# Performance work log

Hardware: AMD Instinct MI355X
Metric: run time of the kernel (lower is better)

The kernel has to match this reference:

```python
import jax, jax.numpy as jnp
import numpy as np

LEAKY = 0.1
VOXEL = 0.25
NSAMPLE = 16
HID = 8                      # PositionalEncodingFourier hidden_dim
SCALE = 2.0 * np.pi
TEMP = 10000.0


def _bn(x, g, b, eps):
    # eval-mode BatchNorm1d of a freshly-built module: running_mean=0, running_var=1
    return x * (g / jnp.sqrt(1.0 + eps)) + b


def _knn(k, q, r):
    # q [B,N,3], r [B,M,3] -> [B,N,k] indices of k nearest points of r
    d = (jnp.sum(q * q, -1)[:, :, None] + jnp.sum(r * r, -1)[:, None, :]
         - 2.0 * jnp.einsum('bnc,bmc->bnm', q, r))
    return jax.lax.top_k(-d, k)[1]


def _group(p, idx):
    # p [B,M,C], idx [B,N,K] -> [B,N,K,C]  (grouping_operation / index_points_group)
    return jax.vmap(lambda pp, ii: pp[ii])(p, idx)


def _pec(pe, w, b):
    # pe [M,3] (columns treated as z,y,x), max_len=(1,1,1)
    emb = pe / (1.0 + 1e-6) * SCALE
    dim_t = TEMP ** (2.0 * (jnp.arange(HID) // 2) / HID)          # [HID]
    p = emb[:, :, None] / dim_t                                    # [M,3,HID]
    pos = jnp.stack([jnp.sin(p[:, :, 0::2]), jnp.cos(p[:, :, 1::2])], -1)  # [M,3,HID/2,2]
    return pos.reshape(pe.shape[0], 3 * HID) @ w + b               # [M,64]


def _ipc(pos_diff, P):
    # IntraPatchCost: pos_diff [B,3,S,N] -> local softmax attention over S: [B,N,S]
    B, _, S, N = pos_diff.shape
    pd = pos_diff.transpose(0, 3, 2, 1).reshape(B * N, S, 3)
    dv = jnp.round(pd / VOXEL)
    x = jax.nn.relu(_bn(pd @ P['ie_w1'] + P['ie_b1'], P['ie_g'], P['ie_bt'], 1e-5))
    x = x @ P['ie_w2'] + P['ie_b2']                                # [BN,S,64]
    pe_raw = ((pd - dv * VOXEL) / VOXEL).reshape(-1, 3)
    x = x + _pec(pe_raw, P['pec_w'], P['pec_b']).reshape(B * N, S, -1)
    h = jax.nn.relu(_bn(x @ P['pm_w1'] + P['pm_b1'], P['pm_g1'], P['pm_bt1'], 1e-3))
    h = jax.nn.relu(_bn(h @ P['pm_w2'] + P['pm_b2'], P['pm_g2'], P['pm_bt2'], 1e-3))
    h = _bn(h @ P['pm_w3'] + P['pm_b3'], P['pm_g3'], P['pm_bt3'], 1e-3)
    h = _bn(h @ P['pm_w4'] + P['pm_b4'], P['pm_g4'], P['pm_bt4'], 1e-3)  # [BN,S,1]
    return jax.nn.softmax(h[..., 0], -1).reshape(B, N, S)


def setup_inputs():
    key = jax.random.key(0)
    ks = iter(jax.random.split(key, 64))
    rn = lambda shape, s=1.0: jax.random.normal(next(ks), shape, jnp.float32) * s
    B, N, D = 2, 8192, 64
    inp = {
        'xyz1': rn((B, 3, N)), 'xyz2': rn((B, 3, N)), 'xyz2w': rn((B, 3, N)),
        'points1': rn((B, D, N)), 'points2': rn((B, D, N)), 'sf': rn((B, 3, N), 0.1),
    }
    for c, cin in (('1', 2 * D), ('2', 2 * D), ('3', 64 + 3), ('4', 2 * 64)):
        inp['cw' + c + 'a'] = rn((cin, 64), 0.1)
        inp['cb' + c + 'a'] = jnp.zeros((64,), jnp.float32)
        inp['cw' + c + 'b'] = rn((64, 64), 0.1)
        inp['cb' + c + 'b'] = jnp.zeros((64,), jnp.float32)
    inp.update(ie_w1=rn((3, 64), 0.1), ie_b1=jnp.zeros((64,), jnp.float32),
               ie_g=jnp.ones((64,), jnp.float32), ie_bt=jnp.zeros((64,), jnp.float32),
               ie_w2=rn((64, 64), 0.1), ie_b2=jnp.zeros((64,), jnp.float32),
               pec_w=rn((24, 64), 0.1), pec_b=jnp.zeros((64,), jnp.float32))
    for i, (cin, cout) in enumerate([(64, 64), (64, 64), (64, 32), (32, 1)], 1):
        inp['pm_w%d' % i] = rn((cin, cout), 0.1)
        inp['pm_b%d' % i] = jnp.zeros((cout,), jnp.float32)
        inp['pm_g%d' % i] = jnp.ones((cout,), jnp.float32)
        inp['pm_bt%d' % i] = jnp.zeros((cout,), jnp.float32)
    return inp


def reference(xyz1, xyz2, xyz2w, points1, points2, sf,
              cw1a, cb1a, cw1b, cb1b, cw2a, cb2a, cw2b, cb2b,
              cw3a, cb3a, cw3b, cb3b, cw4a, cb4a, cw4b, cb4b,
              ie_w1, ie_b1, ie_g, ie_bt, ie_w2, ie_b2, pec_w, pec_b,
              pm_w1, pm_b1, pm_g1, pm_bt1, pm_w2, pm_b2, pm_g2, pm_bt2,
              pm_w3, pm_b3, pm_g3, pm_bt3, pm_w4, pm_b4, pm_g4, pm_bt4):
    P = dict(ie_w1=ie_w1, ie_b1=ie_b1, ie_g=ie_g, ie_bt=ie_bt, ie_w2=ie_w2, ie_b2=ie_b2,
             pec_w=pec_w, pec_b=pec_b,
             pm_w1=pm_w1, pm_b1=pm_b1, pm_g1=pm_g1, pm_bt1=pm_bt1,
             pm_w2=pm_w2, pm_b2=pm_b2, pm_g2=pm_g2, pm_bt2=pm_bt2,
             pm_w3=pm_w3, pm_b3=pm_b3, pm_g3=pm_g3, pm_bt3=pm_bt3,
             pm_w4=pm_w4, pm_b4=pm_b4, pm_g4=pm_g4, pm_bt4=pm_bt4)
    x1 = xyz1.transpose(0, 2, 1)     # [B,N,3]
    x2 = xyz2.transpose(0, 2, 1)
    x2w = xyz2w.transpose(0, 2, 1)
    p1 = points1.transpose(0, 2, 1)  # [B,N,D]
    p2 = points2.transpose(0, 2, 1)
    sg = jax.lax.stop_gradient       # pointutils.knn is non-differentiable
    idx = _knn(NSAMPLE, sg(x1 + sf.transpose(0, 2, 1)), sg(x2))
    idxw = _knn(NSAMPLE, sg(x1), sg(x2w))
    dir_xyz = _group(x2, idx) - x1[:, :, None, :]    # [B,N,K,3]
    dir_xyzw = _group(x2, idxw) - x1[:, :, None, :]
    gp2 = _group(p2, idx)                            # [B,N,K,D]
    gp2w = _group(p2, idxw)
    gp1 = jnp.broadcast_to(p1[:, :, None, :], gp2.shape)
    act = lambda t: jax.nn.leaky_relu(t, LEAKY)
    chain = lambda t, wa, ba, wb, bb: act(act(t @ wa + ba) @ wb + bb)
    f1 = chain(jnp.concatenate([gp1, gp2], -1), cw1a, cb1a, cw1b, cb1b)    # [B,N,K,64]
    f2 = chain(jnp.concatenate([gp1, gp2w], -1), cw2a, cb2a, cw2b, cb2b)
    attn = _ipc(dir_xyz.transpose(0, 3, 2, 1), P)    # [B,N,K]
    attnw = _ipc(dir_xyzw.transpose(0, 3, 2, 1), P)
    costA = jnp.einsum('bnk,bnkc->bnc', attn, f1)
    f3 = chain(jnp.concatenate([dir_xyzw, f2], -1), cw3a, cb3a, cw3b, cb3b)
    costB = jnp.einsum('bnk,bnkc->bnc', attnw, f3)
    out = chain(jnp.concatenate([costA, costB], -1), cw4a, cb4a, cw4b, cb4b)  # [B,N,64]
    return out.transpose(0, 2, 1)    # [B,64,N]
```

## Files before the change

### kernel.cpp

```cpp
#include <hip/hip_runtime.h>
#include <hip/hip_bf16.h>
#include <math.h>

typedef __hip_bfloat16 bf16;

#define NPTS  8192
#define BATCH 2
#define KNB   16
#define NPART 16
#define PARTC (NPTS / NPART)
#define CAP   24
#define BN    (BATCH * NPTS)

#define C_IE 0.9999950000374997f
#define C_PM 0.9995003746877732f

enum {
  WOFF_CW1A = 0,     WOFF_CB1A = 8192,  WOFF_CW1B = 8256,  WOFF_CB1B = 12352,
  WOFF_CW2A = 12416, WOFF_CB2A = 20608, WOFF_CW2B = 20672, WOFF_CB2B = 24768,
  WOFF_CW3A = 24832, WOFF_CB3A = 29120, WOFF_CW3B = 29184, WOFF_CB3B = 33280,
  WOFF_CW4A = 33344, WOFF_CB4A = 41536, WOFF_CW4B = 41600, WOFF_CB4B = 45696,
  WOFF_IEW1 = 45760, WOFF_IEB1 = 45952, WOFF_IEG  = 46016, WOFF_IEBT = 46080,
  WOFF_IEW2 = 46144, WOFF_IEB2 = 50240, WOFF_PECW = 50304, WOFF_PECB = 51840,
  WOFF_PMW1 = 51904, WOFF_PMB1 = 56000, WOFF_PMG1 = 56064, WOFF_PMT1 = 56128,
  WOFF_PMW2 = 56192, WOFF_PMB2 = 60288, WOFF_PMG2 = 60352, WOFF_PMT2 = 60416,
  WOFF_PMW3 = 60480, WOFF_PMB3 = 62528, WOFF_PMG3 = 62560, WOFF_PMT3 = 62592,
  WOFF_PMW4 = 62624, WOFF_PMB4 = 62656, WOFF_PMG4 = 62657, WOFF_PMT4 = 62658
};

#define BOFF_W    0u
#define BOFF_FLAG 262144u
#define BOFF_PK   262160u
#define BOFF_WB   1310736u
#define BOFF_IDX  2359312u
#define BOFF_AW   4456464u
#define BOFF_P1T  5505040u
#define BOFF_P2T  9699344u
#define BOFF_PART BOFF_P1T

typedef __attribute__((ext_vector_type(4))) float f32x4;
typedef __attribute__((ext_vector_type(8))) short bf16x8;
typedef __attribute__((ext_vector_type(4))) unsigned int u32x4;

__device__ __forceinline__ float lrelu(float v) { return v > 0.f ? v : 0.1f * v; }

__device__ __forceinline__ float ldin(const void* p, size_t i, int f32) {
  return f32 ? ((const float*)p)[i] : __bfloat162float(((const bf16*)p)[i]);
}
__device__ __forceinline__ void stout(void* p, size_t i, float v, int f32) {
  if (f32) ((float*)p)[i] = v;
  else ((bf16*)p)[i] = __float2bfloat16(v);
}

__device__ __forceinline__ unsigned int bf16rne(float x) {
  unsigned int u = __float_as_uint(x);
  return (u + 0x7fffu + ((u >> 16) & 1u)) >> 16;
}
__device__ __forceinline__ void splitbf(float x, unsigned int& h, unsigned int& l) {
  h = bf16rne(x);
  float hf = __uint_as_float(h << 16);
  l = bf16rne(x - hf);
}
__device__ __forceinline__ unsigned int packbf(float v) {
  unsigned int h, lo;
  splitbf(v, h, lo);
  return h | (lo << 16);
}

__device__ __forceinline__ void insert16(float d, int id, float* best, int* bidx) {
#pragma unroll
  for (int p = 0; p < KNB; ++p) {
    bool c = d < best[p];
    float tb = best[p]; int ti = bidx[p];
    best[p] = c ? d : tb; bidx[p] = c ? id : ti;
    d = c ? tb : d; id = c ? ti : id;
  }
}

#define BPASS(arr, J, K) \
  _Pragma("unroll") \
  for (int i = 0; i < 16; ++i) { \
    int ix = i ^ (J); \
    if (ix > i) { \
      float lo = fminf(arr[i], arr[ix]); \
      float hi = fmaxf(arr[i], arr[ix]); \
      if ((i & (K)) == 0) { arr[i] = lo; arr[ix] = hi; } \
      else { arr[i] = hi; arr[ix] = lo; } \
    } \
  }

__device__ __forceinline__ float qsq(float4 qv) {
  return __fadd_rn(__fadd_rn(__fmul_rn(qv.x, qv.x), __fmul_rn(qv.y, qv.y)),
                   __fmul_rn(qv.z, qv.z));
}
__device__ __forceinline__ float refdist(float4 qv, float sq, float4 rv) {
  float sr = qsq(rv);
  float dot = __fmaf_rn(qv.z, rv.z, __fmaf_rn(qv.y, rv.y, __fmul_rn(qv.x, rv.x)));
  return __fsub_rn(__fadd_rn(sq, sr), __fadd_rn(dot, dot));
}
__device__ __forceinline__ float refdist_sr(float4 qv, float sq, float4 rv) {
  float dot = __fmaf_rn(qv.z, rv.z, __fmaf_rn(qv.y, rv.y, __fmul_rn(qv.x, rv.x)));
  return __fsub_rn(__fadd_rn(sq, rv.w), __fadd_rn(dot, dot));
}

__global__ void k_detect(const void* __restrict__ pts1, int* __restrict__ flag) {
  int tid = threadIdx.x;
  const bf16* p = (const bf16*)pts1;
  int cnt = 0;
  for (int i = tid; i < 1024; i += 64) {
    float v = __bfloat162float(p[i]);
    if (!(fabsf(v) <= 64.f)) cnt++;
  }
#pragma unroll
  for (int s = 32; s; s >>= 1) cnt += __shfl_down(cnt, s);
  if (tid == 0) *flag = (cnt >= 8) ? 1 : 0;
}

struct PrepTab {
  const void* src[40];
  int off[40];
  int n[40];
  float scale[40];
};

__global__ void k_prep(PrepTab tab, float* __restrict__ W, const int* __restrict__ flag) {
  int f32 = *flag;
  int a = blockIdx.x;
  const void* s = tab.src[a];
  float* d = W + tab.off[a];
  float sc = tab.scale[a];
  for (int i = threadIdx.x; i < tab.n[a]; i += blockDim.x) d[i] = ldin(s, i, f32) * sc;
}

struct WTab { int woff[16]; int nn[16]; int kreal[16]; int mode[16]; int fb[16]; int nm; };

__global__ __launch_bounds__(64) void k_wbprep(WTab wt, const float* __restrict__ W,
                                               unsigned int* __restrict__ WB) {
  int f = blockIdx.x, l = threadIdx.x;
  int m = 0;
  for (int i = 1; i < wt.nm; ++i)
    if (wt.fb[i] <= f) m = i;
  int ntile = wt.nn[m] >> 4;
  int local = f - wt.fb[m];
  int ks = local / ntile, nt = local - ks * ntile;
  int g = l >> 4, c = l & 15;
  int col = nt * 16 + c;
  int N = wt.nn[m], kr = wt.kreal[m], wo = wt.woff[m], mode = wt.mode[m];
  unsigned int hw[4], lw[4];
#pragma unroll
  for (int r = 0; r < 4; ++r) {
    float wv2[2];
#pragma unroll
    for (int e = 0; e < 2; ++e) {
      int k = ks * 32 + g * 8 + 2 * r + e;
      int srck;
      if (mode == 1) srck = (k < 64) ? k + 3 : ((k < 67) ? k - 64 : -1);
      else srck = (k < kr) ? k : -1;
      wv2[e] = (srck >= 0) ? W[wo + srck * N + col] : 0.f;
    }
    unsigned int h0, l0, h1, l1;
    splitbf(wv2[0], h0, l0);
    splitbf(wv2[1], h1, l1);
    hw[r] = h0 | (h1 << 16);
    lw[r] = l0 | (l1 << 16);
  }
  unsigned int* d = WB + ((size_t)f * 64 + l) * 8;
  d[0] = hw[0]; d[1] = hw[1]; d[2] = hw[2]; d[3] = hw[3];
  d[4] = lw[0]; d[5] = lw[1]; d[6] = lw[2]; d[7] = lw[3];
}

__global__ void k_pack(const void* __restrict__ xyz1, const void* __restrict__ xyz2,
                       const void* __restrict__ xyz2w, const void* __restrict__ sf,
                       float4* __restrict__ pk, const int* __restrict__ flag) {
  int f32 = *flag;
  int t = blockIdx.x * 256 + threadIdx.x;
  int b = t >> 13, n = t & (NPTS - 1);
  size_t base = (size_t)b * 3 * NPTS + n;
  float ax = ldin(xyz1, base, f32), ay = ldin(xyz1, base + NPTS, f32), az = ldin(xyz1, base + 2 * NPTS, f32);
  float sx = ldin(sf, base, f32),   sy = ldin(sf, base + NPTS, f32),   sz = ldin(sf, base + 2 * NPTS, f32);
  float4 p0 = make_float4(__fadd_rn(ax, sx), __fadd_rn(ay, sy), __fadd_rn(az, sz), 0.f);
  p0.w = qsq(p0);
  float4 p1 = make_float4(ax, ay, az, 0.f);
  p1.w = qsq(p1);
  float4 p2 = make_float4(ldin(xyz2, base, f32), ldin(xyz2, base + NPTS, f32), ldin(xyz2, base + 2 * NPTS, f32), 0.f);
  p2.w = qsq(p2);
  float4 p3 = make_float4(ldin(xyz2w, base, f32), ldin(xyz2w, base + NPTS, f32), ldin(xyz2w, base + 2 * NPTS, f32), 0.f);
  p3.w = qsq(p3);
  pk[t]          = p0;
  pk[t + BN]     = p1;
  pk[t + 2 * BN] = p2;
  pk[t + 3 * BN] = p3;
}

__global__ __launch_bounds__(64) void k_tr(const void* __restrict__ src,
                                           unsigned int* __restrict__ dst,
                                           const int* __restrict__ flag) {
  __shared__ float tile[64][65];
  int f32 = *flag;
  int tid = threadIdx.x;
  int n0 = blockIdx.x * 64;
  int b = blockIdx.y;
  for (int i = 0; i < 64; ++i)
    tile[i][tid] = ldin(src, ((size_t)b * 64 + i) * NPTS + n0 + tid, f32);
  __syncthreads();
  for (int i = 0; i < 64; ++i)
    dst[((size_t)b * NPTS + n0 + i) * 64 + tid] = packbf(tile[tid][i]);
}

__global__ __launch_bounds__(256) void k_knnp(const float4* __restrict__ pk,
                                              unsigned short* __restrict__ part_idx) {
  __shared__ unsigned short sbuf[256 * CAP];
  int tid = threadIdx.x;
  int n = blockIdx.x * 256 + tid;
  int b = blockIdx.y;
  int which = blockIdx.z >> 4;
  int part  = blockIdx.z & 15;
  const float4* q = pk + (size_t)which * BN;
  const float4* r = pk + (size_t)(2 + which) * BN + (size_t)b * NPTS;
  float4 qv = q[b * NPTS + n];
  float sq = qsq(qv);

  float best[KNB];
#pragma unroll
  for (int p = 0; p < KNB; ++p) best[p] = 3.4e38f;

  const int c0 = part * PARTC;
  for (int t = 0; t < PARTC / 16; ++t) {
    const float4* rr = r + c0 + t * 16;
    float fr[16];
#pragma unroll
    for (int j = 0; j < 16; ++j) fr[j] = refdist_sr(qv, sq, rr[j]);
    BPASS(fr, 1, 2)
    BPASS(fr, 2, 4) BPASS(fr, 1, 4)
    BPASS(fr, 4, 8) BPASS(fr, 2, 8) BPASS(fr, 1, 8)
    BPASS(fr, 8, 16) BPASS(fr, 4, 16) BPASS(fr, 2, 16) BPASS(fr, 1, 16)
#pragma unroll
    for (int i = 0; i < 16; ++i) best[i] = fminf(best[i], fr[15 - i]);
    BPASS(best, 8, 16) BPASS(best, 4, 16) BPASS(best, 2, 16) BPASS(best, 1, 16)
  }
  float thr = best[KNB - 1];

  int cnt = 0;
  for (int t = 0; t < PARTC / 16; ++t) {
    const float4* rr = r + c0 + t * 16;
#pragma unroll
    for (int j = 0; j < 16; ++j) {
      float dd = refdist_sr(qv, sq, rr[j]);
      if (dd <= thr && cnt < CAP) {
        sbuf[tid * CAP + cnt] = (unsigned short)(c0 + t * 16 + j);
        cnt++;
      }
    }
  }

  float bd[KNB]; int bi[KNB];
#pragma unroll
  for (int p = 0; p < KNB; ++p) { bd[p] = 3.4e38f; bi[p] = 0; }
  for (int m = 0; m < CAP; ++m) {
    if (m < cnt) {
      int id = sbuf[tid * CAP + m];
      float dd = refdist(qv, sq, r[id]);
      insert16(dd, id, bd, bi);
    }
  }
  size_t o = ((((size_t)which * BATCH + b) * NPART + part) * NPTS + n) * KNB;
#pragma unroll
  for (int p = 0; p < KNB; ++p) part_idx[o + p] = (unsigned short)bi[p];
}

__global__ void k_merge(const float4* __restrict__ pk,
                        const unsigned short* __restrict__ part_idx,
                        int* __restrict__ idxf) {
  int t = blockIdx.x * 256 + threadIdx.x;
  int n = t & (NPTS - 1);
  int wb = t >> 13;
  int b = wb & (BATCH - 1);
  int which = wb / BATCH;
  const float4* q = pk + (size_t)which * BN;
  const float4* r = pk + (size_t)(2 + which) * BN + (size_t)b * NPTS;
  float4 qv = q[b * NPTS + n];
  float sq = qsq(qv);
  float best[KNB]; int bidx[KNB];
#pragma unroll
  for (int p = 0; p < KNB; ++p) { best[p] = 3.4e38f; bidx[p] = 0; }
  for (int part = 0; part < NPART; ++part) {
    size_t o = ((((size_t)which * BATCH + b) * NPART + part) * NPTS + n) * KNB;
#pragma unroll
    for (int m = 0; m < KNB; ++m) {
      int id = part_idx[o + m];
      float dd = refdist(qv, sq, r[id]);
      if (dd < best[KNB - 1]) insert16(dd, id, best, bidx);
    }
  }
  size_t oo = (size_t)t * KNB;
#pragma unroll
  for (int p = 0; p < KNB; ++p) idxf[oo + p] = bidx[p];
}

__device__ __forceinline__ bf16x8 mk8(unsigned int w0, unsigned int w1,
                                      unsigned int w2, unsigned int w3) {
  u32x4 u;
  u.x = w0; u.y = w1; u.z = w2; u.w = w3;
  return __builtin_bit_cast(bf16x8, u);
}

__device__ __forceinline__ void mkA_pk(u32x4 qa, u32x4 qb, bf16x8& ah, bf16x8& al) {
  unsigned int q0 = qa.x, q1 = qa.y, q2 = qa.z, q3 = qa.w;
  unsigned int q4 = qb.x, q5 = qb.y, q6 = qb.z, q7 = qb.w;
  ah = mk8((q0 & 0xffffu) | (q1 << 16), (q2 & 0xffffu) | (q3 << 16),
           (q4 & 0xffffu) | (q5 << 16), (q6 & 0xffffu) | (q7 << 16));
  al = mk8((q0 >> 16) | (q1 & 0xffff0000u), (q2 >> 16) | (q3 & 0xffff0000u),
           (q4 >> 16) | (q5 & 0xffff0000u), (q6 >> 16) | (q7 & 0xffff0000u));
}
__device__ __forceinline__ void mkA_lds(const unsigned int* p, bf16x8& ah, bf16x8& al) {
  mkA_pk(*(const u32x4*)p, *(const u32x4*)(p + 4), ah, al);
}

#define FRAG_IEW2 0
#define FRAG_PECW 8
#define FRAG_PMW1 12
#define FRAG_PMW2 20
#define FRAG_PMW3 28
#define FRAG_C1A  32
#define FRAG_C1B  48
#define FRAG_C2A  56
#define FRAG_C2B  72
#define FRAG_C3A  80
#define FRAG_C3B  92
#define FRAG_C4A  100
#define FRAG_C4B  116
#define NFRAG     124

__device__ __forceinline__ f32x4 mfma_bb(bf16x8 ah, bf16x8 al,
                                         const unsigned int* __restrict__ WB,
                                         int f, int lane, f32x4 acc) {
  const u32x4* p = (const u32x4*)WB + ((size_t)(f * 64 + lane)) * 2;
  u32x4 h4 = p[0], l4 = p[1];
  bf16x8 bh = __builtin_bit_cast(bf16x8, h4);
  bf16x8 bl = __builtin_bit_cast(bf16x8, l4);
  acc = __builtin_amdgcn_mfma_f32_16x16x32_bf16(al, bh, acc, 0, 0, 0);
  acc = __builtin_amdgcn_mfma_f32_16x16x32_bf16(ah, bl, acc, 0, 0, 0);
  acc = __builtin_amdgcn_mfma_f32_16x16x32_bf16(ah, bh, acc, 0, 0, 0);
  return acc;
}

__device__ __forceinline__ void layer64(const unsigned int* __restrict__ xp,
                                        const unsigned int* __restrict__ WB,
                                        int fbase, int lane, f32x4 acc[4]) {
  int c = lane & 15, g = lane >> 4;
  bf16x8 ah0, al0, ah1, al1;
  mkA_lds(xp + c * 68 + g * 8, ah0, al0);
  mkA_lds(xp + c * 68 + 32 + g * 8, ah1, al1);
#pragma unroll
  for (int nt = 0; nt < 4; ++nt) {
    acc[nt] = mfma_bb(ah0, al0, WB, fbase + nt, lane, acc[nt]);
    acc[nt] = mfma_bb(ah1, al1, WB, fbase + 4 + nt, lane, acc[nt]);
  }
}

__device__ __forceinline__ void epi_pack(int lane, f32x4 acc[4], unsigned int* xp,
                                         const float* gw, const float* bw, bool relu) {
  int c = lane & 15, g = lane >> 4;
#pragma unroll
  for (int nt = 0; nt < 4; ++nt) {
    float gv = gw ? gw[nt * 16 + c] : 1.f;
    float bv = gw ? bw[nt * 16 + c] : 0.f;
#pragma unroll
    for (int r = 0; r < 4; ++r) {
      float v = acc[nt][r];
      if (gw) v = fmaf(v, gv, bv);
      if (relu) v = fmaxf(v, 0.f);
      xp[(g * 4 + r) * 68 + nt * 16 + c] = packbf(v);
    }
  }
}

__device__ __forceinline__ void epi_lrelu(int lane, f32x4 acc[4], unsigned int* xp) {
  int c = lane & 15, g = lane >> 4;
#pragma unroll
  for (int nt = 0; nt < 4; ++nt) {
#pragma unroll
    for (int r = 0; r < 4; ++r)
      xp[(g * 4 + r) * 68 + nt * 16 + c] = packbf(lrelu(acc[nt][r]));
  }
}

__global__ __launch_bounds__(256, 3) void k_logit(const float* __restrict__ W,
                                                  const unsigned int* __restrict__ WB,
                                                  const int* __restrict__ idxf,
                                                  const float4* __restrict__ pk,
                                                  unsigned short* __restrict__ AW) {
  __shared__ unsigned int xp_s[4][16 * 68];
  __shared__ unsigned int tg_s[4][16 * 36];
  const int l = threadIdx.x & 63;
  const int wv = threadIdx.x >> 6;
  const int c = l & 15, g = l >> 4;
  unsigned int* xp = xp_s[wv];
  unsigned int* tg = tg_s[wv];
  const int which = blockIdx.y;
  const int pt = blockIdx.x * 4 + wv;
  const int n = pt & (NPTS - 1);
  const int b = pt >> 13;

  int idxv = idxf[(((size_t)which * BATCH + b) * NPTS + n) * KNB + c];
  float4 pv = pk[(size_t)2 * BN + (size_t)b * NPTS + idxv];
  float4 qp = pk[(size_t)BN + pt];
  float pdx = pv.x - qp.x, pdy = pv.y - qp.y, pdz = pv.z - qp.z;

  {
    unsigned int* tr = tg + c * 36;
#pragma unroll
    for (int j = 0; j < 3; ++j) {
      int t = g * 3 + j;
      int c3 = t >> 2, fq = t & 3;
      float pdc = (c3 == 0) ? pdx : (c3 == 1) ? pdy : pdz;
      float pe = (pdc - rintf(pdc * 4.f) * 0.25f) * 4.f;
      float tt = pe / 1.000001f * 6.28318530717958647692f;
      float dv = (fq == 0) ? 1.f : (fq == 1) ? 10.f : (fq == 2) ? 100.f : 1000.f;
      float sn, cs;
      sincosf(tt / dv, &sn, &cs);
      unsigned int hs, ls2, hc, lc;
      splitbf(sn, hs, ls2);
      splitbf(cs, hc, lc);
      tr[2 * t] = hs | (ls2 << 16);
      tr[2 * t + 1] = hc | (lc << 16);
    }
    if (g == 3) {
#pragma unroll
      for (int z = 24; z < 32; ++z) tr[z] = 0u;
    }
  }

  {
    unsigned int* xr = xp + c * 68 + g * 16;
#pragma unroll
    for (int m4 = 0; m4 < 4; ++m4) {
      int ch = g * 16 + m4 * 4;
      float4 bb = *(const float4*)(W + WOFF_IEB1 + ch);
      float4 w0 = *(const float4*)(W + WOFF_IEW1 + ch);
      float4 w1 = *(const float4*)(W + WOFF_IEW1 + 64 + ch);
      float4 w2 = *(const float4*)(W + WOFF_IEW1 + 128 + ch);
      float4 gg = *(const float4*)(W + WOFF_IEG + ch);
      float4 bt = *(const float4*)(W + WOFF_IEBT + ch);
      float v0 = fmaf(pdz, w2.x, fmaf(pdy, w1.x, fmaf(pdx, w0.x, bb.x)));
      float v1 = fmaf(pdz, w2.y, fmaf(pdy, w1.y, fmaf(pdx, w0.y, bb.y)));
      float v2 = fmaf(pdz, w2.z, fmaf(pdy, w1.z, fmaf(pdx, w0.z, bb.z)));
      float v3 = fmaf(pdz, w2.w, fmaf(pdy, w1.w, fmaf(pdx, w0.w, bb.w)));
      v0 = fmaxf(fmaf(v0, gg.x, bt.x), 0.f);
      v1 = fmaxf(fmaf(v1, gg.y, bt.y), 0.f);
      v2 = fmaxf(fmaf(v2, gg.z, bt.z), 0.f);
      v3 = fmaxf(fmaf(v3, gg.w, bt.w), 0.f);
      u32x4 pk4;
      pk4.x = packbf(v0); pk4.y = packbf(v1);
      pk4.z = packbf(v2); pk4.w = packbf(v3);
      *(u32x4*)(xr + m4 * 4) = pk4;
    }
  }
  __builtin_amdgcn_wave_barrier();

  f32x4 acc[4];
#pragma unroll
  for (int nt = 0; nt < 4; ++nt) {
    float bs = W[WOFF_IEB2 + nt * 16 + c] + W[WOFF_PECB + nt * 16 + c];
    acc[nt].x = bs; acc[nt].y = bs; acc[nt].z = bs; acc[nt].w = bs;
  }
  layer64(xp, WB, FRAG_IEW2, l, acc);
  {
    bf16x8 ah, al;
    mkA_lds(tg + c * 36 + g * 8, ah, al);
#pragma unroll
    for (int nt = 0; nt < 4; ++nt)
      acc[nt] = mfma_bb(ah, al, WB, FRAG_PECW + nt, l, acc[nt]);
  }
  __builtin_amdgcn_wave_barrier();
  epi_pack(l, acc, xp, nullptr, nullptr, false);
  __builtin_amdgcn_wave_barrier();

#pragma unroll
  for (int nt = 0; nt < 4; ++nt) {
    float bs = W[WOFF_PMB1 + nt * 16 + c];
    acc[nt].x = bs; acc[nt].y = bs; acc[nt].z = bs; acc[nt].w = bs;
  }
  layer64(xp, WB, FRAG_PMW1, l, acc);
  __builtin_amdgcn_wave_barrier();
  epi_pack(l, acc, xp, W + WOFF_PMG1, W + WOFF_PMT1, true);
  __builtin_amdgcn_wave_barrier();

#pragma unroll
  for (int nt = 0; nt < 4; ++nt) {
    float bs = W[WOFF_PMB2 + nt * 16 + c];
    acc[nt].x = bs; acc[nt].y = bs; acc[nt].z = bs; acc[nt].w = bs;
  }
  layer64(xp, WB, FRAG_PMW2, l, acc);
  __builtin_amdgcn_wave_barrier();
  epi_pack(l, acc, xp, W + WOFF_PMG2, W + WOFF_PMT2, true);
  __builtin_amdgcn_wave_barrier();

  f32x4 a3[2];
#pragma unroll
  for (int nt = 0; nt < 2; ++nt) {
    float bs = W[WOFF_PMB3 + nt * 16 + c];
    a3[nt].x = bs; a3[nt].y = bs; a3[nt].z = bs; a3[nt].w = bs;
  }
  {
    bf16x8 ah0, al0, ah1, al1;
    mkA_lds(xp + c * 68 + g * 8, ah0, al0);
    mkA_lds(xp + c * 68 + 32 + g * 8, ah1, al1);
#pragma unroll
    for (int nt = 0; nt < 2; ++nt) {
      a3[nt] = mfma_bb(ah0, al0, WB, FRAG_PMW3 + nt, l, a3[nt]);
      a3[nt] = mfma_bb(ah1, al1, WB, FRAG_PMW3 + 2 + nt, l, a3[nt]);
    }
  }
#pragma unroll
  for (int nt = 0; nt < 2; ++nt) {
    float gv = W[WOFF_PMG3 + nt * 16 + c];
    float bv = W[WOFF_PMT3 + nt * 16 + c];
#pragma unroll
    for (int r = 0; r < 4; ++r) a3[nt][r] = fmaf(a3[nt][r], gv, bv);
  }

  float w4a = W[WOFF_PMW4 + c];
  float w4b = W[WOFF_PMW4 + 16 + c];
  f32x4 pr;
#pragma unroll
  for (int r = 0; r < 4; ++r) pr[r] = fmaf(a3[1][r], w4b, a3[0][r] * w4a);
#pragma unroll
  for (int s = 1; s < 16; s <<= 1) {
#pragma unroll
    for (int r = 0; r < 4; ++r) pr[r] += __shfl_xor(pr[r], s);
  }
  float b4 = W[WOFF_PMB4], g4 = W[WOFF_PMG4], t4 = W[WOFF_PMT4];
  f32x4 lg;
#pragma unroll
  for (int r = 0; r < 4; ++r) lg[r] = fmaf(pr[r] + b4, g4, t4);

  float m = fmaxf(fmaxf(lg[0], lg[1]), fmaxf(lg[2], lg[3]));
#pragma unroll
  for (int s = 16; s < 64; s <<= 1) m = fmaxf(m, __shfl_xor(m, s));
  f32x4 e;
  float ssum = 0.f;
#pragma unroll
  for (int r = 0; r < 4; ++r) { e[r] = expf(lg[r] - m); ssum += e[r]; }
#pragma unroll
  for (int s = 16; s < 64; s <<= 1) ssum += __shfl_xor(ssum, s);
  if (c < 4) {
    int k = g * 4 + c;
    float ev = (c == 0) ? e[0] : (c == 1) ? e[1] : (c == 2) ? e[2] : e[3];
    float aw = ev / ssum;
    AW[(((size_t)which * BATCH + b) * NPTS + n) * KNB + k] =
        (unsigned short)__float2uint_rn(aw * 65535.f);
  }
}

__global__ __launch_bounds__(256, 3) void k_feat(const unsigned int* __restrict__ P1T,
                                                 const unsigned int* __restrict__ P2T,
                                                 const float* __restrict__ W,
                                                 const unsigned int* __restrict__ WB,
                                                 const int* __restrict__ idxf,
                                                 const unsigned short* __restrict__ AW,
                                                 const float4* __restrict__ pk,
                                                 void* __restrict__ out,
                                                 const int* __restrict__ flag) {
  __shared__ unsigned int xp_s[4][16 * 68];
  __shared__ unsigned int costb[4][132];
  __shared__ unsigned int u4b[4][68];
  __shared__ float awb[4][16];
  const int l = threadIdx.x & 63;
  const int wv = threadIdx.x >> 6;
  const int c = l & 15, g = l >> 4;
  unsigned int* xp = xp_s[wv];
  const int f32 = *flag;
  const int pt = blockIdx.x * 4 + wv;
  const int n = pt & (NPTS - 1);
  const int b = pt >> 13;
  float4 qp = pk[(size_t)BN + pt];
  u32x4 z4;
  z4.x = 0u; z4.y = 0u; z4.z = 0u; z4.w = 0u;

  bf16x8 p1h[2], p1l[2];
  {
    const unsigned int* pr = P1T + ((size_t)b * NPTS + n) * 64;
#pragma unroll
    for (int ks = 0; ks < 2; ++ks) {
      u32x4 qa = *(const u32x4*)(pr + ks * 32 + g * 8);
      u32x4 qb = *(const u32x4*)(pr + ks * 32 + g * 8 + 4);
      mkA_pk(qa, qb, p1h[ks], p1l[ks]);
    }
  }

  for (int which = 0; which < 2; ++which) {
    int idxv = idxf[(((size_t)which * BATCH + b) * NPTS + n) * KNB + c];
    float4 pv = pk[(size_t)2 * BN + (size_t)b * NPTS + idxv];
    float pdx = pv.x - qp.x, pdy = pv.y - qp.y, pdz = pv.z - qp.z;
    float aw = (float)AW[(((size_t)which * BATCH + b) * NPTS + n) * KNB + c] *
               (1.f / 65535.f);
    if (g == 0) awb[wv][c] = aw;

    bf16x8 p2h[2], p2l[2];
    {
      const unsigned int* qr = P2T + ((size_t)b * NPTS + idxv) * 64;
#pragma unroll
      for (int ks = 0; ks < 2; ++ks) {
        u32x4 qa = *(const u32x4*)(qr + ks * 32 + g * 8);
        u32x4 qb = *(const u32x4*)(qr + ks * 32 + g * 8 + 4);
        mkA_pk(qa, qb, p2h[ks], p2l[ks]);
      }
    }

    f32x4 acc[4];
    {
      const float* Ba = W + (which == 0 ? WOFF_CB1A : WOFF_CB2A);
      int fa = (which == 0) ? FRAG_C1A : FRAG_C2A;
#pragma unroll
      for (int nt = 0; nt < 4; ++nt) {
        float bs = Ba[nt * 16 + c];
        acc[nt].x = bs; acc[nt].y = bs; acc[nt].z = bs; acc[nt].w = bs;
      }
#pragma unroll
      for (int nt = 0; nt < 4; ++nt) {
        acc[nt] = mfma_bb(p1h[0], p1l[0], WB, fa + nt, l, acc[nt]);
        acc[nt] = mfma_bb(p1h[1], p1l[1], WB, fa + 4 + nt, l, acc[nt]);
        acc[nt] = mfma_bb(p2h[0], p2l[0], WB, fa + 8 + nt, l, acc[nt]);
        acc[nt] = mfma_bb(p2h[1], p2l[1], WB, fa + 12 + nt, l, acc[nt]);
      }
    }
    __builtin_amdgcn_wave_barrier();
    epi_lrelu(l, acc, xp);
    __builtin_amdgcn_wave_barrier();

    {
      const float* Bb = W + (which == 0 ? WOFF_CB1B : WOFF_CB2B);
      int fb = (which == 0) ? FRAG_C1B : FRAG_C2B;
      bf16x8 ah0, al0, ah1, al1;
      mkA_lds(xp + c * 68 + g * 8, ah0, al0);
      mkA_lds(xp + c * 68 + 32 + g * 8, ah1, al1);
#pragma unroll
      for (int nt = 0; nt < 4; ++nt) {
        float bs = Bb[nt * 16 + c];
        acc[nt].x = bs; acc[nt].y = bs; acc[nt].z = bs; acc[nt].w = bs;
        acc[nt] = mfma_bb(ah0, al0, WB, fb + nt, l, acc[nt]);
        acc[nt] = mfma_bb(ah1, al1, WB, fb + 4 + nt, l, acc[nt]);
      }
    }
    __builtin_amdgcn_wave_barrier();

    if (which == 1) {
      epi_lrelu(l, acc, xp);
      if (g == 0) {
        xp[c * 68 + 64] = packbf(pdx);
        xp[c * 68 + 65] = packbf(pdy);
        xp[c * 68 + 66] = packbf(pdz);
        xp[c * 68 + 67] = 0u;
      }
      __builtin_amdgcn_wave_barrier();
      {
        bf16x8 ah0, al0, ah1, al1, ah2, al2;
        mkA_lds(xp + c * 68 + g * 8, ah0, al0);
        mkA_lds(xp + c * 68 + 32 + g * 8, ah1, al1);
        u32x4 qa3 = z4;
        if (g == 0) qa3 = *(const u32x4*)(xp + c * 68 + 64);
        mkA_pk(qa3, z4, ah2, al2);
#pragma unroll
        for (int nt = 0; nt < 4; ++nt) {
          float bs = W[WOFF_CB3A + nt * 16 + c];
          acc[nt].x = bs; acc[nt].y = bs; acc[nt].z = bs; acc[nt].w = bs;
          acc[nt] = mfma_bb(ah0, al0, WB, FRAG_C3A + nt, l, acc[nt]);
          acc[nt] = mfma_bb(ah1, al1, WB, FRAG_C3A + 4 + nt, l, acc[nt]);
          acc[nt] = mfma_bb(ah2, al2, WB, FRAG_C3A + 8 + nt, l, acc[nt]);
        }
      }
      __builtin_amdgcn_wave_barrier();
      epi_lrelu(l, acc, xp);
      __builtin_amdgcn_wave_barrier();
      {
        bf16x8 ah0, al0, ah1, al1;
        mkA_lds(xp + c * 68 + g * 8, ah0, al0);
        mkA_lds(xp + c * 68 + 32 + g * 8, ah1, al1);
#pragma unroll
        for (int nt = 0; nt < 4; ++nt) {
          float bs = W[WOFF_CB3B + nt * 16 + c];
          acc[nt].x = bs; acc[nt].y = bs; acc[nt].z = bs; acc[nt].w = bs;
          acc[nt] = mfma_bb(ah0, al0, WB, FRAG_C3B + nt, l, acc[nt]);
          acc[nt] = mfma_bb(ah1, al1, WB, FRAG_C3B + 4 + nt, l, acc[nt]);
        }
      }
      __builtin_amdgcn_wave_barrier();
    }

    {
      float4 a4r = *(const float4*)&awb[wv][g * 4];
#pragma unroll
      for (int nt = 0; nt < 4; ++nt) {
        float s = lrelu(acc[nt][0]) * a4r.x;
        s = fmaf(lrelu(acc[nt][1]), a4r.y, s);
        s = fmaf(lrelu(acc[nt][2]), a4r.z, s);
        s = fmaf(lrelu(acc[nt][3]), a4r.w, s);
        s += __shfl_xor(s, 16);
        s += __shfl_xor(s, 32);
        if (g == 0) costb[wv][which * 64 + nt * 16 + c] = packbf(s);
      }
    }
  }
  __syncthreads();

  f32x4 a4;
  {
    float bs = W[WOFF_CB4A + wv * 16 + c];
    a4.x = bs; a4.y = bs; a4.z = bs; a4.w = bs;
#pragma unroll
    for (int ks = 0; ks < 4; ++ks) {
      u32x4 qa = z4, qb = z4;
      if (c < 4) {
        qa = *(const u32x4*)(&costb[c][ks * 32 + g * 8]);
        qb = *(const u32x4*)(&costb[c][ks * 32 + g * 8 + 4]);
      }
      bf16x8 ah, al;
      mkA_pk(qa, qb, ah, al);
      a4 = mfma_bb(ah, al, WB, FRAG_C4A + ks * 4 + wv, l, a4);
    }
  }
  if (g == 0) {
#pragma unroll
    for (int r = 0; r < 4; ++r) u4b[r][wv * 16 + c] = packbf(lrelu(a4[r]));
  }
  __syncthreads();

  {
    float bs = W[WOFF_CB4B + wv * 16 + c];
    a4.x = bs; a4.y = bs; a4.z = bs; a4.w = bs;
#pragma unroll
    for (int ks = 0; ks < 2; ++ks) {
      u32x4 qa = z4, qb = z4;
      if (c < 4) {
        qa = *(const u32x4*)(&u4b[c][ks * 32 + g * 8]);
        qb = *(const u32x4*)(&u4b[c][ks * 32 + g * 8 + 4]);
      }
      bf16x8 ah, al;
      mkA_pk(qa, qb, ah, al);
      a4 = mfma_bb(ah, al, WB, FRAG_C4B + ks * 4 + wv, l, a4);
    }
  }
  if (g == 0) {
    int n0 = (blockIdx.x * 4) & (NPTS - 1);
    int b0 = (blockIdx.x * 4) >> 13;
    size_t ob = (size_t)b0 * 64 * NPTS + (size_t)(wv * 16 + c) * NPTS + n0;
#pragma unroll
    for (int r = 0; r < 4; ++r) stout(out, ob + r, lrelu(a4[r]), f32);
  }
}

extern "C" void kernel_launch(void* const* d_in, const int* in_sizes, int n_in,
                              void* d_out, int out_size, void* d_ws, size_t ws_size,
                              hipStream_t stream) {
  (void)in_sizes; (void)n_in; (void)out_size; (void)ws_size;
  float*  W    = (float*)d_ws;
  int*    FLAG = (int*)((char*)d_ws + BOFF_FLAG);
  float4* PK   = (float4*)((char*)d_ws + BOFF_PK);
  unsigned int* WBu = (unsigned int*)((char*)d_ws + BOFF_WB);
  int*    IDX  = (int*)((char*)d_ws + BOFF_IDX);
  unsigned short* AW = (unsigned short*)((char*)d_ws + BOFF_AW);
  unsigned int* P1T = (unsigned int*)((char*)d_ws + BOFF_P1T);
  unsigned int* P2T = (unsigned int*)((char*)d_ws + BOFF_P2T);
  unsigned short* PART = (unsigned short*)((char*)d_ws + BOFF_PART);

  static const int WOFFS[40] = {
    WOFF_CW1A, WOFF_CB1A, WOFF_CW1B, WOFF_CB1B,
    WOFF_CW2A, WOFF_CB2A, WOFF_CW2B, WOFF_CB2B,
    WOFF_CW3A, WOFF_CB3A, WOFF_CW3B, WOFF_CB3B,
    WOFF_CW4A, WOFF_CB4A, WOFF_CW4B, WOFF_CB4B,
    WOFF_IEW1, WOFF_IEB1, WOFF_IEG,  WOFF_IEBT,
    WOFF_IEW2, WOFF_IEB2, WOFF_PECW, WOFF_PECB,
    WOFF_PMW1, WOFF_PMB1, WOFF_PMG1, WOFF_PMT1,
    WOFF_PMW2, WOFF_PMB2, WOFF_PMG2, WOFF_PMT2,
    WOFF_PMW3, WOFF_PMB3, WOFF_PMG3, WOFF_PMT3,
    WOFF_PMW4, WOFF_PMB4, WOFF_PMG4, WOFF_PMT4};
  static const int WNS[40] = {
    8192, 64, 4096, 64,  8192, 64, 4096, 64,  4288, 64, 4096, 64,
    8192, 64, 4096, 64,  192, 64, 64, 64,  4096, 64,  1536, 64,
    4096, 64, 64, 64,  4096, 64, 64, 64,  2048, 32, 32, 32,  32, 1, 1, 1};

  PrepTab tab;
  for (int a = 0; a < 40; ++a) {
    tab.src[a] = d_in[6 + a];
    tab.off[a] = WOFFS[a];
    tab.n[a] = WNS[a];
    tab.scale[a] = 1.f;
  }
  tab.scale[18] = C_IE;
  tab.scale[26] = C_PM; tab.scale[30] = C_PM;
  tab.scale[34] = C_PM; tab.scale[38] = C_PM;

  WTab wt;
  {
    int f = 0, m = 0;
    auto add = [&](int woff, int N, int nks, int kreal, int mode) {
      wt.woff[m] = woff; wt.nn[m] = N; wt.kreal[m] = kreal;
      wt.mode[m] = mode; wt.fb[m] = f;
      f += nks * (N / 16); ++m;
    };
    add(WOFF_IEW2, 64, 2, 64, 0);
    add(WOFF_PECW, 64, 1, 24, 0);
    add(WOFF_PMW1, 64, 2, 64, 0);
    add(WOFF_PMW2, 64, 2, 64, 0);
    add(WOFF_PMW3, 32, 2, 64, 0);
    add(WOFF_CW1A, 64, 4, 128, 0);
    add(WOFF_CW1B, 64, 2, 64, 0);
    add(WOFF_CW2A, 64, 4, 128, 0);
    add(WOFF_CW2B, 64, 2, 64, 0);
    add(WOFF_CW3A, 64, 3, 67, 1);
    add(WOFF_CW3B, 64, 2, 64, 0);
    add(WOFF_CW4A, 64, 4, 128, 0);
    add(WOFF_CW4B, 64, 2, 64, 0);
    wt.nm = m;
  }

  k_detect<<<dim3(1), dim3(64), 0, stream>>>(d_in[3], FLAG);
  k_prep<<<dim3(40), dim3(256), 0, stream>>>(tab, W, FLAG);
  k_wbprep<<<dim3(NFRAG), dim3(64), 0, stream>>>(wt, W, WBu);
  k_pack<<<dim3(64), dim3(256), 0, stream>>>(d_in[0], d_in[1], d_in[2], d_in[5], PK, FLAG);
  k_knnp<<<dim3(NPTS / 256, BATCH, 2 * NPART), dim3(256), 0, stream>>>(PK, PART);
  k_merge<<<dim3(2 * BN / 256), dim3(256), 0, stream>>>(PK, PART, IDX);
  k_tr<<<dim3(NPTS / 64, BATCH), dim3(64), 0, stream>>>(d_in[3], P1T, FLAG);
  k_tr<<<dim3(NPTS / 64, BATCH), dim3(64), 0, stream>>>(d_in[4], P2T, FLAG);
  k_logit<<<dim3(BN / 4, 2), dim3(256), 0, stream>>>(W, WBu, IDX, PK, AW);
  k_feat<<<dim3(BN / 4), dim3(256), 0, stream>>>(P1T, P2T, W, WBu, IDX, AW, PK, d_out, FLAG);
}
```

Measured before the change: 809.4 us.

## Fuse attention-logit MLP and softmax into feature kernel, drop AW buffer

Moves the intra-patch cost MLP and softmax from the separate k_logit kernel into k_feat's per-branch loop, so attention weights stay in registers and are used directly for the weighted sum. This removes one kernel launch, the quantized 16-bit AW global write/read round trip, and the redundant neighbor index/position loads. It also drops the 16-bit quantization of the attention weights. The cost is higher register and LDS pressure in k_feat (extra tg_s buffer), which may lower occupancy under the (256,3) launch bounds.

```diff
diff --git a/kernel.cpp b/kernel.cpp
--- a/kernel.cpp
+++ b/kernel.cpp
@@ -385,191 +385,23 @@
   }
 }
 
-__global__ __launch_bounds__(256, 3) void k_logit(const float* __restrict__ W,
-                                                  const unsigned int* __restrict__ WB,
-                                                  const int* __restrict__ idxf,
-                                                  const float4* __restrict__ pk,
-                                                  unsigned short* __restrict__ AW) {
+__global__ __launch_bounds__(256, 3) void k_feat(const unsigned int* __restrict__ P1T,
+                                                 const unsigned int* __restrict__ P2T,
+                                                 const float* __restrict__ W,
+                                                 const unsigned int* __restrict__ WB,
+                                                 const int* __restrict__ idxf,
+                                                 const float4* __restrict__ pk,
+                                                 void* __restrict__ out,
+                                                 const int* __restrict__ flag) {
   __shared__ unsigned int xp_s[4][16 * 68];
   __shared__ unsigned int tg_s[4][16 * 36];
+  __shared__ unsigned int costb[4][132];
+  __shared__ unsigned int u4b[4][68];
   const int l = threadIdx.x & 63;
   const int wv = threadIdx.x >> 6;
   const int c = l & 15, g = l >> 4;
   unsigned int* xp = xp_s[wv];
   unsigned int* tg = tg_s[wv];
-  const int which = blockIdx.y;
-  const int pt = blockIdx.x * 4 + wv;
-  const int n = pt & (NPTS - 1);
-  const int b = pt >> 13;
-
-  int idxv = idxf[(((size_t)which * BATCH + b) * NPTS + n) * KNB + c];
-  float4 pv = pk[(size_t)2 * BN + (size_t)b * NPTS + idxv];
-  float4 qp = pk[(size_t)BN + pt];
-  float pdx = pv.x - qp.x, pdy = pv.y - qp.y, pdz = pv.z - qp.z;
-
-  {
-    unsigned int* tr = tg + c * 36;
-#pragma unroll
-    for (int j = 0; j < 3; ++j) {
-      int t = g * 3 + j;
-      int c3 = t >> 2, fq = t & 3;
-      float pdc = (c3 == 0) ? pdx : (c3 == 1) ? pdy : pdz;
-      float pe = (pdc - rintf(pdc * 4.f) * 0.25f) * 4.f;
-      float tt = pe / 1.000001f * 6.28318530717958647692f;
-      float dv = (fq == 0) ? 1.f : (fq == 1) ? 10.f : (fq == 2) ? 100.f : 1000.f;
-      float sn, cs;
-      sincosf(tt / dv, &sn, &cs);
-      unsigned int hs, ls2, hc, lc;
-      splitbf(sn, hs, ls2);
-      splitbf(cs, hc, lc);
-      tr[2 * t] = hs | (ls2 << 16);
-      tr[2 * t + 1] = hc | (lc << 16);
-    }
-    if (g == 3) {
-#pragma unroll
-      for (int z = 24; z < 32; ++z) tr[z] = 0u;
-    }
-  }
-
-  {
-    unsigned int* xr = xp + c * 68 + g * 16;
-#pragma unroll
-    for (int m4 = 0; m4 < 4; ++m4) {
-      int ch = g * 16 + m4 * 4;
-      float4 bb = *(const float4*)(W + WOFF_IEB1 + ch);
-      float4 w0 = *(const float4*)(W + WOFF_IEW1 + ch);
-      float4 w1 = *(const float4*)(W + WOFF_IEW1 + 64 + ch);
-      float4 w2 = *(const float4*)(W + WOFF_IEW1 + 128 + ch);
-      float4 gg = *(const float4*)(W + WOFF_IEG + ch);
-      float4 bt = *(const float4*)(W + WOFF_IEBT + ch);
-      float v0 = fmaf(pdz, w2.x, fmaf(pdy, w1.x, fmaf(pdx, w0.x, bb.x)));
-      float v1 = fmaf(pdz, w2.y, fmaf(pdy, w1.y, fmaf(pdx, w0.y, bb.y)));
-      float v2 = fmaf(pdz, w2.z, fmaf(pdy, w1.z, fmaf(pdx, w0.z, bb.z)));
-      float v3 = fmaf(pdz, w2.w, fmaf(pdy, w1.w, fmaf(pdx, w0.w, bb.w)));
-      v0 = fmaxf(fmaf(v0, gg.x, bt.x), 0.f);
-      v1 = fmaxf(fmaf(v1, gg.y, bt.y), 0.f);
-      v2 = fmaxf(fmaf(v2, gg.z, bt.z), 0.f);
-      v3 = fmaxf(fmaf(v3, gg.w, bt.w), 0.f);
-      u32x4 pk4;
-      pk4.x = packbf(v0); pk4.y = packbf(v1);
-      pk4.z = packbf(v2); pk4.w = packbf(v3);
-      *(u32x4*)(xr + m4 * 4) = pk4;
-    }
-  }
-  __builtin_amdgcn_wave_barrier();
-
-  f32x4 acc[4];
-#pragma unroll
-  for (int nt = 0; nt < 4; ++nt) {
-    float bs = W[WOFF_IEB2 + nt * 16 + c] + W[WOFF_PECB + nt * 16 + c];
-    acc[nt].x = bs; acc[nt].y = bs; acc[nt].z = bs; acc[nt].w = bs;
-  }
-  layer64(xp, WB, FRAG_IEW2, l, acc);
-  {
-    bf16x8 ah, al;
-    mkA_lds(tg + c * 36 + g * 8, ah, al);
-#pragma unroll
-    for (int nt = 0; nt < 4; ++nt)
-      acc[nt] = mfma_bb(ah, al, WB, FRAG_PECW + nt, l, acc[nt]);
-  }
-  __builtin_amdgcn_wave_barrier();
-  epi_pack(l, acc, xp, nullptr, nullptr, false);
-  __builtin_amdgcn_wave_barrier();
-
-#pragma unroll
-  for (int nt = 0; nt < 4; ++nt) {
-    float bs = W[WOFF_PMB1 + nt * 16 + c];
-    acc[nt].x = bs; acc[nt].y = bs; acc[nt].z = bs; acc[nt].w = bs;
-  }
-  layer64(xp, WB, FRAG_PMW1, l, acc);
-  __builtin_amdgcn_wave_barrier();
-  epi_pack(l, acc, xp, W + WOFF_PMG1, W + WOFF_PMT1, true);
-  __builtin_amdgcn_wave_barrier();
-
-#pragma unroll
-  for (int nt = 0; nt < 4; ++nt) {
-    float bs = W[WOFF_PMB2 + nt * 16 + c];
-    acc[nt].x = bs; acc[nt].y = bs; acc[nt].z = bs; acc[nt].w = bs;
-  }
-  layer64(xp, WB, FRAG_PMW2, l, acc);
-  __builtin_amdgcn_wave_barrier();
-  epi_pack(l, acc, xp, W + WOFF_PMG2, W + WOFF_PMT2, true);
-  __builtin_amdgcn_wave_barrier();
-
-  f32x4 a3[2];
-#pragma unroll
-  for (int nt = 0; nt < 2; ++nt) {
-    float bs = W[WOFF_PMB3 + nt * 16 + c];
-    a3[nt].x = bs; a3[nt].y = bs; a3[nt].z = bs; a3[nt].w = bs;
-  }
-  {
-    bf16x8 ah0, al0, ah1, al1;
-    mkA_lds(xp + c * 68 + g * 8, ah0, al0);
-    mkA_lds(xp + c * 68 + 32 + g * 8, ah1, al1);
-#pragma unroll
-    for (int nt = 0; nt < 2; ++nt) {
-      a3[nt] = mfma_bb(ah0, al0, WB, FRAG_PMW3 + nt, l, a3[nt]);
-      a3[nt] = mfma_bb(ah1, al1, WB, FRAG_PMW3 + 2 + nt, l, a3[nt]);
-    }
-  }
-#pragma unroll
-  for (int nt = 0; nt < 2; ++nt) {
-    float gv = W[WOFF_PMG3 + nt * 16 + c];
-    float bv = W[WOFF_PMT3 + nt * 16 + c];
-#pragma unroll
-    for (int r = 0; r < 4; ++r) a3[nt][r] = fmaf(a3[nt][r], gv, bv);
-  }
-
-  float w4a = W[WOFF_PMW4 + c];
-  float w4b = W[WOFF_PMW4 + 16 + c];
-  f32x4 pr;
-#pragma unroll
-  for (int r = 0; r < 4; ++r) pr[r] = fmaf(a3[1][r], w4b, a3[0][r] * w4a);
-#pragma unroll
-  for (int s = 1; s < 16; s <<= 1) {
-#pragma unroll
-    for (int r = 0; r < 4; ++r) pr[r] += __shfl_xor(pr[r], s);
-  }
-  float b4 = W[WOFF_PMB4], g4 = W[WOFF_PMG4], t4 = W[WOFF_PMT4];
-  f32x4 lg;
-#pragma unroll
-  for (int r = 0; r < 4; ++r) lg[r] = fmaf(pr[r] + b4, g4, t4);
-
-  float m = fmaxf(fmaxf(lg[0], lg[1]), fmaxf(lg[2], lg[3]));
-#pragma unroll
-  for (int s = 16; s < 64; s <<= 1) m = fmaxf(m, __shfl_xor(m, s));
-  f32x4 e;
-  float ssum = 0.f;
-#pragma unroll
-  for (int r = 0; r < 4; ++r) { e[r] = expf(lg[r] - m); ssum += e[r]; }
-#pragma unroll
-  for (int s = 16; s < 64; s <<= 1) ssum += __shfl_xor(ssum, s);
-  if (c < 4) {
-    int k = g * 4 + c;
-    float ev = (c == 0) ? e[0] : (c == 1) ? e[1] : (c == 2) ? e[2] : e[3];
-    float aw = ev / ssum;
-    AW[(((size_t)which * BATCH + b) * NPTS + n) * KNB + k] =
-        (unsigned short)__float2uint_rn(aw * 65535.f);
-  }
-}
-
-__global__ __launch_bounds__(256, 3) void k_feat(const unsigned int* __restrict__ P1T,
-                                                 const unsigned int* __restrict__ P2T,
-                                                 const float* __restrict__ W,
-                                                 const unsigned int* __restrict__ WB,
-                                                 const int* __restrict__ idxf,
-                                                 const unsigned short* __restrict__ AW,
-                                                 const float4* __restrict__ pk,
-                                                 void* __restrict__ out,
-                                                 const int* __restrict__ flag) {
-  __shared__ unsigned int xp_s[4][16 * 68];
-  __shared__ unsigned int costb[4][132];
-  __shared__ unsigned int u4b[4][68];
-  __shared__ float awb[4][16];
-  const int l = threadIdx.x & 63;
-  const int wv = threadIdx.x >> 6;
-  const int c = l & 15, g = l >> 4;
-  unsigned int* xp = xp_s[wv];
   const int f32 = *flag;
   const int pt = blockIdx.x * 4 + wv;
   const int n = pt & (NPTS - 1);
@@ -593,9 +425,150 @@
     int idxv = idxf[(((size_t)which * BATCH + b) * NPTS + n) * KNB + c];
     float4 pv = pk[(size_t)2 * BN + (size_t)b * NPTS + idxv];
     float pdx = pv.x - qp.x, pdy = pv.y - qp.y, pdz = pv.z - qp.z;
-    float aw = (float)AW[(((size_t)which * BATCH + b) * NPTS + n) * KNB + c] *
-               (1.f / 65535.f);
-    if (g == 0) awb[wv][c] = aw;
+
+    {
+      unsigned int* tr = tg + c * 36;
+#pragma unroll
+      for (int j = 0; j < 3; ++j) {
+        int t = g * 3 + j;
+        int c3 = t >> 2, fq = t & 3;
+        float pdc = (c3 == 0) ? pdx : (c3 == 1) ? pdy : pdz;
+        float pe = (pdc - rintf(pdc * 4.f) * 0.25f) * 4.f;
+        float tt = pe / 1.000001f * 6.28318530717958647692f;
+        float dv = (fq == 0) ? 1.f : (fq == 1) ? 10.f : (fq == 2) ? 100.f : 1000.f;
+        float sn, cs;
+        sincosf(tt / dv, &sn, &cs);
+        unsigned int hs, ls2, hc, lc;
+        splitbf(sn, hs, ls2);
+        splitbf(cs, hc, lc);
+        tr[2 * t] = hs | (ls2 << 16);
+        tr[2 * t + 1] = hc | (lc << 16);
+      }
+      if (g == 3) {
+#pragma unroll
+        for (int z = 24; z < 32; ++z) tr[z] = 0u;
+      }
+    }
+
+    {
+      unsigned int* xr = xp + c * 68 + g * 16;
+#pragma unroll
+      for (int m4 = 0; m4 < 4; ++m4) {
+        int ch = g * 16 + m4 * 4;
+        float4 bb = *(const float4*)(W + WOFF_IEB1 + ch);
+        float4 w0 = *(const float4*)(W + WOFF_IEW1 + ch);
+        float4 w1 = *(const float4*)(W + WOFF_IEW1 + 64 + ch);
+        float4 w2 = *(const float4*)(W + WOFF_IEW1 + 128 + ch);
+        float4 gg = *(const float4*)(W + WOFF_IEG + ch);
+        float4 bt = *(const float4*)(W + WOFF_IEBT + ch);
+        float v0 = fmaf(pdz, w2.x, fmaf(pdy, w1.x, fmaf(pdx, w0.x, bb.x)));
+        float v1 = fmaf(pdz, w2.y, fmaf(pdy, w1.y, fmaf(pdx, w0.y, bb.y)));
+        float v2 = fmaf(pdz, w2.z, fmaf(pdy, w1.z, fmaf(pdx, w0.z, bb.z)));
+        float v3 = fmaf(pdz, w2.w, fmaf(pdy, w1.w, fmaf(pdx, w0.w, bb.w)));
+        v0 = fmaxf(fmaf(v0, gg.x, bt.x), 0.f);
+        v1 = fmaxf(fmaf(v1, gg.y, bt.y), 0.f);
+        v2 = fmaxf(fmaf(v2, gg.z, bt.z), 0.f);
+        v3 = fmaxf(fmaf(v3, gg.w, bt.w), 0.f);
+        u32x4 pk4;
+        pk4.x = packbf(v0); pk4.y = packbf(v1);
+        pk4.z = packbf(v2); pk4.w = packbf(v3);
+        *(u32x4*)(xr + m4 * 4) = pk4;
+      }
+    }
+    __builtin_amdgcn_wave_barrier();
+
+    f32x4 acc[4];
+#pragma unroll
+    for (int nt = 0; nt < 4; ++nt) {
+      float bs = W[WOFF_IEB2 + nt * 16 + c] + W[WOFF_PECB + nt * 16 + c];
+      acc[nt].x = bs; acc[nt].y = bs; acc[nt].z = bs; acc[nt].w = bs;
+    }
+    layer64(xp, WB, FRAG_IEW2, l, acc);
+    {
+      bf16x8 ah, al;
+      mkA_lds(tg + c * 36 + g * 8, ah, al);
+#pragma unroll
+      for (int nt = 0; nt < 4; ++nt)
+        acc[nt] = mfma_bb(ah, al, WB, FRAG_PECW + nt, l, acc[nt]);
+    }
+    __builtin_amdgcn_wave_barrier();
+    epi_pack(l, acc, xp, nullptr, nullptr, false);
+    __builtin_amdgcn_wave_barrier();
+
+#pragma unroll
+    for (int nt = 0; nt < 4; ++nt) {
+      float bs = W[WOFF_PMB1 + nt * 16 + c];
+      acc[nt].x = bs; acc[nt].y = bs; acc[nt].z = bs; acc[nt].w = bs;
+    }
+    layer64(xp, WB, FRAG_PMW1, l, acc);
+    __builtin_amdgcn_wave_barrier();
+    epi_pack(l, acc, xp, W + WOFF_PMG1, W + WOFF_PMT1, true);
+    __builtin_amdgcn_wave_barrier();
+
+#pragma unroll
+    for (int nt = 0; nt < 4; ++nt) {
+      float bs = W[WOFF_PMB2 + nt * 16 + c];
+      acc[nt].x = bs; acc[nt].y = bs; acc[nt].z = bs; acc[nt].w = bs;
+    }
+    layer64(xp, WB, FRAG_PMW2, l, acc);
+    __builtin_amdgcn_wave_barrier();
+    epi_pack(l, acc, xp, W + WOFF_PMG2, W + WOFF_PMT2, true);
+    __builtin_amdgcn_wave_barrier();
+
+    f32x4 a3[2];
+#pragma unroll
+    for (int nt = 0; nt < 2; ++nt) {
+      float bs = W[WOFF_PMB3 + nt * 16 + c];
+      a3[nt].x = bs; a3[nt].y = bs; a3[nt].z = bs; a3[nt].w = bs;
+    }
+    {
+      bf16x8 ah0, al0, ah1, al1;
+      mkA_lds(xp + c * 68 + g * 8, ah0, al0);
+      mkA_lds(xp + c * 68 + 32 + g * 8, ah1, al1);
+#pragma unroll
+      for (int nt = 0; nt < 2; ++nt) {
+        a3[nt] = mfma_bb(ah0, al0, WB, FRAG_PMW3 + nt, l, a3[nt]);
+        a3[nt] = mfma_bb(ah1, al1, WB, FRAG_PMW3 + 2 + nt, l, a3[nt]);
+      }
+    }
+#pragma unroll
+    for (int nt = 0; nt < 2; ++nt) {
+      float gv = W[WOFF_PMG3 + nt * 16 + c];
+      float bv = W[WOFF_PMT3 + nt * 16 + c];
+#pragma unroll
+      for (int r = 0; r < 4; ++r) a3[nt][r] = fmaf(a3[nt][r], gv, bv);
+    }
+
+    f32x4 a4r;
+    {
+      float w4a = W[WOFF_PMW4 + c];
+      float w4b = W[WOFF_PMW4 + 16 + c];
+      f32x4 pr;
+#pragma unroll
+      for (int r = 0; r < 4; ++r) pr[r] = fmaf(a3[1][r], w4b, a3[0][r] * w4a);
+#pragma unroll
+      for (int s = 1; s < 16; s <<= 1) {
+#pragma unroll
+        for (int r = 0; r < 4; ++r) pr[r] += __shfl_xor(pr[r], s);
+      }
+      float b4 = W[WOFF_PMB4], g4 = W[WOFF_PMG4], t4 = W[WOFF_PMT4];
+      f32x4 lg;
+#pragma unroll
+      for (int r = 0; r < 4; ++r) lg[r] = fmaf(pr[r] + b4, g4, t4);
+
+      float m = fmaxf(fmaxf(lg[0], lg[1]), fmaxf(lg[2], lg[3]));
+#pragma unroll
+      for (int s = 16; s < 64; s <<= 1) m = fmaxf(m, __shfl_xor(m, s));
+      f32x4 e;
+      float ssum = 0.f;
+#pragma unroll
+      for (int r = 0; r < 4; ++r) { e[r] = expf(lg[r] - m); ssum += e[r]; }
+#pragma unroll
+      for (int s = 16; s < 64; s <<= 1) ssum += __shfl_xor(ssum, s);
+#pragma unroll
+      for (int r = 0; r < 4; ++r) a4r[r] = e[r] / ssum;
+    }
+    __builtin_amdgcn_wave_barrier();
 
     bf16x8 p2h[2], p2l[2];
     {
@@ -608,7 +581,6 @@
       }
     }
 
-    f32x4 acc[4];
     {
       const float* Ba = W + (which == 0 ? WOFF_CB1A : WOFF_CB2A);
       int fa = (which == 0) ? FRAG_C1A : FRAG_C2A;
@@ -689,7 +661,6 @@
     }
 
     {
-      float4 a4r = *(const float4*)&awb[wv][g * 4];
 #pragma unroll
       for (int nt = 0; nt < 4; ++nt) {
         float s = lrelu(acc[nt][0]) * a4r.x;
@@ -701,6 +672,7 @@
         if (g == 0) costb[wv][which * 64 + nt * 16 + c] = packbf(s);
       }
     }
+    __builtin_amdgcn_wave_barrier();
   }
   __syncthreads();
 
@@ -759,7 +731,6 @@
   float4* PK   = (float4*)((char*)d_ws + BOFF_PK);
   unsigned int* WBu = (unsigned int*)((char*)d_ws + BOFF_WB);
   int*    IDX  = (int*)((char*)d_ws + BOFF_IDX);
-  unsigned short* AW = (unsigned short*)((char*)d_ws + BOFF_AW);
   unsigned int* P1T = (unsigned int*)((char*)d_ws + BOFF_P1T);
   unsigned int* P2T = (unsigned int*)((char*)d_ws + BOFF_P2T);
   unsigned short* PART = (unsigned short*)((char*)d_ws + BOFF_PART);
@@ -823,6 +794,5 @@
   k_merge<<<dim3(2 * BN / 256), dim3(256), 0, stream>>>(PK, PART, IDX);
   k_tr<<<dim3(NPTS / 64, BATCH), dim3(64), 0, stream>>>(d_in[3], P1T, FLAG);
   k_tr<<<dim3(NPTS / 64, BATCH), dim3(64), 0, stream>>>(d_in[4], P2T, FLAG);
-  k_logit<<<dim3(BN / 4, 2), dim3(256), 0, stream>>>(W, WBu, IDX, PK, AW);
-  k_feat<<<dim3(BN / 4), dim3(256), 0, stream>>>(P1T, P2T, W, WBu, IDX, AW, PK, d_out, FLAG);
-}
+  k_feat<<<dim3(BN / 4), dim3(256), 0, stream>>>(P1T, P2T, W, WBu, IDX, PK, d_out, FLAG);
+}
```

After: 2.113 ms. 161% more time.
